# Performance work log

Hardware: AMD Instinct MI355X
Metric: run time of the kernel (lower is better)

Reference implementation:

```python
import jax, jax.numpy as jnp
import numpy as np

B, D = 4096, 512
N_PROTO = 1000          # prototype tasks
CLS_PER_TASK = 10       # indices*10 block size in original code
N_CLASSES = N_PROTO * CLS_PER_TASK
NUM_TEST = 10


def setup_inputs() -> dict:
    key = jax.random.key(0)
    k1, k2, k3 = jax.random.split(key, 3)
    img = jax.random.normal(k1, (B, D), dtype=jnp.float32)
    # image encoder output is L2-normalized and detached in the original
    image_features = img / jnp.linalg.norm(img, axis=-1, keepdims=True)
    ima_proto = jax.random.normal(k2, (N_PROTO, D), dtype=jnp.float32)
    ima_proto = ima_proto / jnp.linalg.norm(ima_proto, axis=-1, keepdims=True)
    text_features_raw = jax.random.normal(k3, (N_CLASSES, D), dtype=jnp.float32)
    logit_scale = jnp.asarray(np.log(1.0 / 0.07), dtype=jnp.float32)  # CLIP init
    return {
        "image_features": image_features,
        "ima_proto": ima_proto,
        "text_features_raw": text_features_raw,
        "logit_scale": logit_scale,
        "num_test": NUM_TEST,
    }


def reference(image_features, ima_proto, text_features_raw, logit_scale, num_test):
    n_proto = ima_proto.shape[0]
    n_classes = text_features_raw.shape[0]
    b = image_features.shape[0]
    k = min(int(num_test), n_proto)

    # probability = image_features @ ima_proto.t(); topk indices
    probability = image_features @ ima_proto.T                      # [B, n_proto]
    _, indices = jax.lax.top_k(probability, k)                      # [B, k]

    # text_features normalized, logit = image_features @ text_features.t()
    text_features = text_features_raw / jnp.linalg.norm(
        text_features_raw, axis=-1, keepdims=True)
    logit = image_features @ text_features.T                        # [B, n_classes]

    # vectorized form of the double loop:
    #   logits[j][idx*10 : idx*10+10] = logit[j][idx*10 : idx*10+10]
    sel = jnp.zeros((b, n_proto), dtype=logit.dtype)
    sel = sel.at[jnp.arange(b)[:, None], indices].set(1.0)          # [B, n_proto]
    block_of_class = jnp.arange(n_classes) // CLS_PER_TASK          # [n_classes]
    mask = sel[:, block_of_class]                                   # [B, n_classes]

    logits = jnp.exp(logit_scale) * (logit * mask)
    return logits
```

## Files before the change

kernel.cpp:

```cpp
#include <hip/hip_runtime.h>
#include <cfloat>
#include <math.h>

#define B_ROWS   4096
#define DIM      512
#define NPROTO   1000
#define NCLASSES 10000
#define KSEL     10
#define KCAND    12
#define CAP      256
#define PROB_LD  1024

#define PROB_BYTES 8388608u
#define OUT_BYTES  163840000u
#define ZHI_N4     ((OUT_BYTES - PROB_BYTES) / 16)
#define ZQ1        6000000u
#define ZS1        0u
#define ZQ2        (ZHI_N4 - ZQ1)
#define ZS2        ZQ1

#define GBM 64
#define GBN 128
#define GBK 32
#define ALD 40

typedef short s16x8 __attribute__((ext_vector_type(8)));
typedef float f32x4 __attribute__((ext_vector_type(4)));

static __device__ __forceinline__ unsigned short f2bf(float f) {
  unsigned int x = __float_as_uint(f);
  return (unsigned short)((x + 0x7fffu + ((x >> 16) & 1u)) >> 16);
}
static __device__ __forceinline__ s16x8 cvt8(float4 a, float4 b) {
  s16x8 r;
  r[0]=f2bf(a.x); r[1]=f2bf(a.y); r[2]=f2bf(a.z); r[3]=f2bf(a.w);
  r[4]=f2bf(b.x); r[5]=f2bf(b.y); r[6]=f2bf(b.z); r[7]=f2bf(b.w);
  return r;
}
static __device__ __forceinline__ unsigned short f2h(float f) {
  _Float16 h = (_Float16)f;
  return __builtin_bit_cast(unsigned short, h);
}

static __device__ __forceinline__ unsigned mono16(unsigned h) {
  return (h & 0x8000u) ? (~h & 0xffffu) : (h | 0x8000u);
}

static __device__ __forceinline__ void zero_share(
    f32x4* __restrict__ zhi, unsigned start, unsigned count,
    unsigned gth, unsigned nthreads)
{
  const f32x4 z4 = (f32x4)0.f;
  for (unsigned i = start + gth; i < start + count; i += nthreads)
    __builtin_nontemporal_store(z4, zhi + i);
}

__global__ __launch_bounds__(256) void k_gemm(
    const float* __restrict__ img, const float* __restrict__ proto,
    unsigned short* __restrict__ prob, f32x4* __restrict__ zhi,
    int* __restrict__ counts)
{
  __shared__ short Al[GBM * ALD];
  __shared__ short Bl[GBN * ALD];

  const int tid  = threadIdx.x;
  const int lane = tid & 63, wave = tid >> 6;
  const int wr = wave >> 1, wc = wave & 1;
  const int row0 = blockIdx.x * GBM;
  const int col0 = blockIdx.y * GBN;
  const unsigned gth = (blockIdx.y * gridDim.x + blockIdx.x) * 256 + tid;

  const int sr = tid >> 2;
  const int sc = (tid & 3) * 8;

  int pa = col0 + sr;      if (pa > NPROTO - 1) pa = NPROTO - 1;
  int pb = col0 + 64 + sr; if (pb > NPROTO - 1) pb = NPROTO - 1;
  const float* gA  = img   + (size_t)(row0 + sr) * DIM + sc;
  const float* gB0 = proto + (size_t)pa * DIM + sc;
  const float* gB1 = proto + (size_t)pb * DIM + sc;

  float4 ra0  = *(const float4*)(gA);      float4 ra1  = *(const float4*)(gA + 4);
  float4 rb00 = *(const float4*)(gB0);     float4 rb01 = *(const float4*)(gB0 + 4);
  float4 rb10 = *(const float4*)(gB1);     float4 rb11 = *(const float4*)(gB1 + 4);

  f32x4 acc[2][4];
#pragma unroll
  for (int m = 0; m < 2; ++m)
#pragma unroll
    for (int n = 0; n < 4; ++n) acc[m][n] = (f32x4)0.f;

  const int kg = lane >> 4;
  const int fr = lane & 15;

  for (int kt = 0; kt < DIM / GBK; ++kt) {
    *(s16x8*)&Al[sr * ALD + sc]        = cvt8(ra0, ra1);
    *(s16x8*)&Bl[sr * ALD + sc]        = cvt8(rb00, rb01);
    *(s16x8*)&Bl[(64 + sr) * ALD + sc] = cvt8(rb10, rb11);
    __syncthreads();

    if (kt + 1 < DIM / GBK) {
      const int k0 = (kt + 1) * GBK;
      ra0  = *(const float4*)(gA + k0);   ra1  = *(const float4*)(gA + k0 + 4);
      rb00 = *(const float4*)(gB0 + k0);  rb01 = *(const float4*)(gB0 + k0 + 4);
      rb10 = *(const float4*)(gB1 + k0);  rb11 = *(const float4*)(gB1 + k0 + 4);
    }

    s16x8 af[2], bf[4];
#pragma unroll
    for (int m = 0; m < 2; ++m)
      af[m] = *(const s16x8*)&Al[(wr * 32 + m * 16 + fr) * ALD + kg * 8];
#pragma unroll
    for (int n = 0; n < 4; ++n)
      bf[n] = *(const s16x8*)&Bl[(wc * 64 + n * 16 + fr) * ALD + kg * 8];
#pragma unroll
    for (int m = 0; m < 2; ++m)
#pragma unroll
      for (int n = 0; n < 4; ++n)
        acc[m][n] = __builtin_amdgcn_mfma_f32_16x16x32_bf16(
            af[m], bf[n], acc[m][n], 0, 0, 0);
    __syncthreads();
  }

#pragma unroll
  for (int m = 0; m < 2; ++m)
#pragma unroll
    for (int n = 0; n < 4; ++n) {
      const int r = row0 + wr * 32 + m * 16 + (lane >> 4) * 4;
      const int c = col0 + wc * 64 + n * 16 + fr;
#pragma unroll
      for (int reg = 0; reg < 4; ++reg)
        prob[(size_t)(r + reg) * PROB_LD + c] = f2h(acc[m][n][reg]);
    }

  if (blockIdx.x == 0 && blockIdx.y == 0)
    for (int i = tid; i < NPROTO; i += 256) counts[i] = 0;

  zero_share(zhi, ZS1, ZQ1, gth, 512 * 256);
}

__global__ __launch_bounds__(256) void k_select(
    unsigned short* __restrict__ prob, const float* __restrict__ img,
    const float* __restrict__ proto, int* __restrict__ counts,
    int* __restrict__ buckets, f32x4* __restrict__ zhi)
{
  const int tid  = threadIdx.x;
  const int wave = tid >> 6, lane = tid & 63;
  const int row  = blockIdx.x * 4 + wave;

  unsigned cand[16];
  {
    const uint4* pu = reinterpret_cast<const uint4*>(
        prob + (size_t)row * PROB_LD) + lane * 2;
    const uint4 w0 = pu[0], w1 = pu[1];
    const unsigned w[8] = {w0.x, w0.y, w0.z, w0.w, w1.x, w1.y, w1.z, w1.w};
    const int cbase = lane * 16;
#pragma unroll
    for (int r = 0; r < 8; ++r) {
      const int c0 = cbase + r * 2;
      const unsigned lo = w[r] & 0xffffu, hi = w[r] >> 16;
      cand[r * 2]     = (c0     < NPROTO) ? ((mono16(lo) << 16) | (0xffffu - c0))       : 0u;
      cand[r * 2 + 1] = (c0 + 1 < NPROTO) ? ((mono16(hi) << 16) | (0xffffu - (c0 + 1))) : 0u;
    }
  }

  int ci[KCAND];
#pragma unroll
  for (int kk = 0; kk < KCAND; ++kk) {
    unsigned best = cand[0];
#pragma unroll
    for (int r = 1; r < 16; ++r) best = max(best, cand[r]);
#pragma unroll
    for (int off = 32; off; off >>= 1)
      best = max(best, (unsigned)__shfl_xor((int)best, off));
    ci[kk] = 0xffff - (int)(best & 0xffffu);
#pragma unroll
    for (int r = 0; r < 16; ++r)
      if (cand[r] == best) cand[r] = 0u;
  }

  {
    const f32x4 z4 = (f32x4)0.f;
    f32x4* prow = reinterpret_cast<f32x4*>(prob + (size_t)row * PROB_LD);
    __builtin_nontemporal_store(z4, prow + lane);
    __builtin_nontemporal_store(z4, prow + 64 + lane);
  }

  const float4* a4 = reinterpret_cast<const float4*>(img + (size_t)row * DIM);
  const float4 a0 = a4[lane], a1 = a4[64 + lane];
  float dv[KCAND];
#pragma unroll
  for (int j = 0; j < KCAND; ++j) {
    const float4* p4 = reinterpret_cast<const float4*>(proto + (size_t)ci[j] * DIM);
    const float4 b0 = p4[lane], b1 = p4[64 + lane];
    float s = 0.f;
    s = fmaf(a0.x, b0.x, s); s = fmaf(a0.y, b0.y, s);
    s = fmaf(a0.z, b0.z, s); s = fmaf(a0.w, b0.w, s);
    s = fmaf(a1.x, b1.x, s); s = fmaf(a1.y, b1.y, s);
    s = fmaf(a1.z, b1.z, s); s = fmaf(a1.w, b1.w, s);
#pragma unroll
    for (int off = 32; off; off >>= 1) s += __shfl_xor(s, off);
    dv[j] = s;
  }

  unsigned picked = 0;
  for (int kk = 0; kk < KSEL; ++kk) {
    float bv = -FLT_MAX;
    int   bj = 0;
#pragma unroll
    for (int j = 0; j < KCAND; ++j)
      if (!((picked >> j) & 1u) && dv[j] > bv) { bv = dv[j]; bj = j; }
    picked |= 1u << bj;
    if (lane == kk) {
      const int pp  = ci[bj];
      const int pos = atomicAdd(&counts[pp], 1);
      if (pos < CAP) buckets[pp * CAP + pos] = row;
    }
  }

  zero_share(zhi, ZS2, ZQ2, blockIdx.x * 256 + tid, 1024 * 256);
}

__global__ __launch_bounds__(256) void k_compute(
    const float* __restrict__ img, const float* __restrict__ text,
    const int* __restrict__ counts, const int* __restrict__ buckets,
    const float* __restrict__ logit_scale, float* __restrict__ out)
{
  __shared__ float stext[KSEL * DIM];
  __shared__ float sfac[KSEL];

  const int p    = blockIdx.x;
  const int tid  = threadIdx.x;
  const int wave = tid >> 6, lane = tid & 63;

  {
    const float4* src = reinterpret_cast<const float4*>(text + (size_t)p * KSEL * DIM);
    float4* dst = reinterpret_cast<float4*>(stext);
#pragma unroll
    for (int i = 0; i < 5; ++i) dst[tid + i * 256] = src[tid + i * 256];
  }
  __syncthreads();

  const float scale = expf(logit_scale[0]);
#pragma unroll
  for (int j = wave; j < KSEL; j += 4) {
    const float4* t4 = reinterpret_cast<const float4*>(stext + j * DIM);
    float4 v0 = t4[lane], v1 = t4[64 + lane];
    float s = 0.f;
    s = fmaf(v0.x, v0.x, s); s = fmaf(v0.y, v0.y, s);
    s = fmaf(v0.z, v0.z, s); s = fmaf(v0.w, v0.w, s);
    s = fmaf(v1.x, v1.x, s); s = fmaf(v1.y, v1.y, s);
    s = fmaf(v1.z, v1.z, s); s = fmaf(v1.w, v1.w, s);
#pragma unroll
    for (int off = 32; off; off >>= 1) s += __shfl_down(s, off);
    if (lane == 0) sfac[j] = scale / sqrtf(s);
  }
  __syncthreads();

  const int n = min(counts[p], CAP);
  const float4* st4 = reinterpret_cast<const float4*>(stext);
  const int* bkt = buckets + p * CAP;

  int row = -1, nrow;
  float4 a0, a1, na0, na1;
  if (wave < n) {
    row = bkt[wave];
    const float4* a4 = reinterpret_cast<const float4*>(img + (size_t)row * DIM);
    a0 = a4[lane]; a1 = a4[64 + lane];
  }

  for (int i = wave; i < n; i += 4) {
    const int inext = i + 4;
    if (inext < n) {
      nrow = bkt[inext];
      const float4* a4 = reinterpret_cast<const float4*>(img + (size_t)nrow * DIM);
      na0 = a4[lane]; na1 = a4[64 + lane];
    }

    float acc[KSEL];
#pragma unroll
    for (int j = 0; j < KSEL; ++j) {
      const float4 b0 = st4[j * 128 + lane];
      const float4 b1 = st4[j * 128 + 64 + lane];
      float s = 0.f;
      s = fmaf(a0.x, b0.x, s); s = fmaf(a0.y, b0.y, s);
      s = fmaf(a0.z, b0.z, s); s = fmaf(a0.w, b0.w, s);
      s = fmaf(a1.x, b1.x, s); s = fmaf(a1.y, b1.y, s);
      s = fmaf(a1.z, b1.z, s); s = fmaf(a1.w, b1.w, s);
      acc[j] = s;
    }
#pragma unroll
    for (int j = 0; j < KSEL; ++j) {
#pragma unroll
      for (int off = 32; off; off >>= 1)
        acc[j] += __shfl_xor(acc[j], off);
    }
    float v = acc[0];
#pragma unroll
    for (int j = 1; j < KSEL; ++j) if (lane == j) v = acc[j];
    if (lane < KSEL)
      out[(size_t)row * NCLASSES + p * KSEL + lane] = v * sfac[lane];

    row = nrow; a0 = na0; a1 = na1;
  }
}

extern "C" void kernel_launch(void* const* d_in, const int* in_sizes, int n_in,
                              void* d_out, int out_size, void* d_ws, size_t ws_size,
                              hipStream_t stream) {
  const float* img    = (const float*)d_in[0];
  const float* proto  = (const float*)d_in[1];
  const float* text   = (const float*)d_in[2];
  const float* lscale = (const float*)d_in[3];

  unsigned short* prob = (unsigned short*)d_out;
  f32x4*  zhi  = (f32x4*)((char*)d_out + PROB_BYTES);
  float*  out  = (float*)d_out;

  int* counts  = (int*)d_ws;
  int* buckets = (int*)((char*)d_ws + 4096);

  k_gemm<<<dim3(B_ROWS / GBM, 1024 / GBN), 256, 0, stream>>>(
      img, proto, prob, zhi, counts);
  k_select<<<B_ROWS / 4, 256, 0, stream>>>(prob, img, proto, counts, buckets, zhi);
  k_compute<<<NPROTO, 256, 0, stream>>>(img, text, counts, buckets, lscale, out);
}
```

Baseline: 99.41 us.

## Fuse prototype GEMM with top-k candidate selection, pre-convert prototypes to bf16

Adds a prep kernel that converts the prototypes to bf16 into a padded workspace buffer and zeroes the counts. The GEMM and top-k selection are merged into one kernel: each 16-row block computes all 1024 prototype scores with MFMA, picks per-wave candidates in registers, merges them through LDS, then reranks in fp32 and fills the buckets. This removes the fp16 probability round-trip through the output buffer and the separate select launch. In exchange each block reads the full bf16 prototype matrix from global/L2 without LDS staging, only 256 blocks are launched, and zeroing the output moves into this one kernel.

```diff
diff --git a/kernel.cpp b/kernel.cpp
--- a/kernel.cpp
+++ b/kernel.cpp
@@ -5,24 +5,13 @@
 #define B_ROWS   4096
 #define DIM      512
 #define NPROTO   1000
+#define NPROTO_P 1024
 #define NCLASSES 10000
 #define KSEL     10
 #define KCAND    12
 #define CAP      256
-#define PROB_LD  1024
-
-#define PROB_BYTES 8388608u
-#define OUT_BYTES  163840000u
-#define ZHI_N4     ((OUT_BYTES - PROB_BYTES) / 16)
-#define ZQ1        6000000u
-#define ZS1        0u
-#define ZQ2        (ZHI_N4 - ZQ1)
-#define ZS2        ZQ1
-
-#define GBM 64
-#define GBN 128
-#define GBK 32
-#define ALD 40
+
+#define OUT_N4   10240000u
 
 typedef short s16x8 __attribute__((ext_vector_type(8)));
 typedef float f32x4 __attribute__((ext_vector_type(4)));
@@ -37,187 +26,156 @@
   r[4]=f2bf(b.x); r[5]=f2bf(b.y); r[6]=f2bf(b.z); r[7]=f2bf(b.w);
   return r;
 }
-static __device__ __forceinline__ unsigned short f2h(float f) {
+static __device__ __forceinline__ unsigned f2h(float f) {
   _Float16 h = (_Float16)f;
-  return __builtin_bit_cast(unsigned short, h);
-}
-
+  return (unsigned)__builtin_bit_cast(unsigned short, h);
+}
 static __device__ __forceinline__ unsigned mono16(unsigned h) {
   return (h & 0x8000u) ? (~h & 0xffffu) : (h | 0x8000u);
 }
 
 static __device__ __forceinline__ void zero_share(
-    f32x4* __restrict__ zhi, unsigned start, unsigned count,
+    f32x4* __restrict__ z, unsigned start, unsigned count,
     unsigned gth, unsigned nthreads)
 {
   const f32x4 z4 = (f32x4)0.f;
   for (unsigned i = start + gth; i < start + count; i += nthreads)
-    __builtin_nontemporal_store(z4, zhi + i);
-}
-
-__global__ __launch_bounds__(256) void k_gemm(
+    __builtin_nontemporal_store(z4, z + i);
+}
+
+__global__ __launch_bounds__(256) void k_prep(
+    const float* __restrict__ proto, short* __restrict__ protb,
+    int* __restrict__ counts)
+{
+  const int u = blockIdx.x * 256 + threadIdx.x;
+  s16x8 r = (s16x8)0;
+  if (u * 8 < NPROTO * DIM) {
+    const float4* s = reinterpret_cast<const float4*>(proto) + (size_t)u * 2;
+    r = cvt8(s[0], s[1]);
+  }
+  *reinterpret_cast<s16x8*>(protb + (size_t)u * 8) = r;
+  if (blockIdx.x == 0)
+    for (int i = threadIdx.x; i < NPROTO; i += 256) counts[i] = 0;
+}
+
+__global__ __launch_bounds__(512) void k_fused(
     const float* __restrict__ img, const float* __restrict__ proto,
-    unsigned short* __restrict__ prob, f32x4* __restrict__ zhi,
-    int* __restrict__ counts)
-{
-  __shared__ short Al[GBM * ALD];
-  __shared__ short Bl[GBN * ALD];
-
-  const int tid  = threadIdx.x;
-  const int lane = tid & 63, wave = tid >> 6;
-  const int wr = wave >> 1, wc = wave & 1;
-  const int row0 = blockIdx.x * GBM;
-  const int col0 = blockIdx.y * GBN;
-  const unsigned gth = (blockIdx.y * gridDim.x + blockIdx.x) * 256 + tid;
-
-  const int sr = tid >> 2;
-  const int sc = (tid & 3) * 8;
-
-  int pa = col0 + sr;      if (pa > NPROTO - 1) pa = NPROTO - 1;
-  int pb = col0 + 64 + sr; if (pb > NPROTO - 1) pb = NPROTO - 1;
-  const float* gA  = img   + (size_t)(row0 + sr) * DIM + sc;
-  const float* gB0 = proto + (size_t)pa * DIM + sc;
-  const float* gB1 = proto + (size_t)pb * DIM + sc;
-
-  float4 ra0  = *(const float4*)(gA);      float4 ra1  = *(const float4*)(gA + 4);
-  float4 rb00 = *(const float4*)(gB0);     float4 rb01 = *(const float4*)(gB0 + 4);
-  float4 rb10 = *(const float4*)(gB1);     float4 rb11 = *(const float4*)(gB1 + 4);
-
-  f32x4 acc[2][4];
-#pragma unroll
-  for (int m = 0; m < 2; ++m)
-#pragma unroll
-    for (int n = 0; n < 4; ++n) acc[m][n] = (f32x4)0.f;
-
-  const int kg = lane >> 4;
-  const int fr = lane & 15;
-
-  for (int kt = 0; kt < DIM / GBK; ++kt) {
-    *(s16x8*)&Al[sr * ALD + sc]        = cvt8(ra0, ra1);
-    *(s16x8*)&Bl[sr * ALD + sc]        = cvt8(rb00, rb01);
-    *(s16x8*)&Bl[(64 + sr) * ALD + sc] = cvt8(rb10, rb11);
-    __syncthreads();
-
-    if (kt + 1 < DIM / GBK) {
-      const int k0 = (kt + 1) * GBK;
-      ra0  = *(const float4*)(gA + k0);   ra1  = *(const float4*)(gA + k0 + 4);
-      rb00 = *(const float4*)(gB0 + k0);  rb01 = *(const float4*)(gB0 + k0 + 4);
-      rb10 = *(const float4*)(gB1 + k0);  rb11 = *(const float4*)(gB1 + k0 + 4);
-    }
-
-    s16x8 af[2], bf[4];
-#pragma unroll
-    for (int m = 0; m < 2; ++m)
-      af[m] = *(const s16x8*)&Al[(wr * 32 + m * 16 + fr) * ALD + kg * 8];
-#pragma unroll
-    for (int n = 0; n < 4; ++n)
-      bf[n] = *(const s16x8*)&Bl[(wc * 64 + n * 16 + fr) * ALD + kg * 8];
-#pragma unroll
-    for (int m = 0; m < 2; ++m)
-#pragma unroll
-      for (int n = 0; n < 4; ++n)
-        acc[m][n] = __builtin_amdgcn_mfma_f32_16x16x32_bf16(
-            af[m], bf[n], acc[m][n], 0, 0, 0);
-    __syncthreads();
-  }
-
-#pragma unroll
-  for (int m = 0; m < 2; ++m)
-#pragma unroll
-    for (int n = 0; n < 4; ++n) {
-      const int r = row0 + wr * 32 + m * 16 + (lane >> 4) * 4;
-      const int c = col0 + wc * 64 + n * 16 + fr;
-#pragma unroll
-      for (int reg = 0; reg < 4; ++reg)
-        prob[(size_t)(r + reg) * PROB_LD + c] = f2h(acc[m][n][reg]);
-    }
-
-  if (blockIdx.x == 0 && blockIdx.y == 0)
-    for (int i = tid; i < NPROTO; i += 256) counts[i] = 0;
-
-  zero_share(zhi, ZS1, ZQ1, gth, 512 * 256);
-}
-
-__global__ __launch_bounds__(256) void k_select(
-    unsigned short* __restrict__ prob, const float* __restrict__ img,
-    const float* __restrict__ proto, int* __restrict__ counts,
-    int* __restrict__ buckets, f32x4* __restrict__ zhi)
-{
+    const short* __restrict__ protb, int* __restrict__ counts,
+    int* __restrict__ buckets, f32x4* __restrict__ outz)
+{
+  __shared__ short A_lds[64 * 128];
+  __shared__ unsigned pool[16][8][KCAND];
+
   const int tid  = threadIdx.x;
   const int wave = tid >> 6, lane = tid & 63;
-  const int row  = blockIdx.x * 4 + wave;
-
-  unsigned cand[16];
+  const int kg = lane >> 4, fr = lane & 15;
+  const int row0 = blockIdx.x * 16;
+
   {
-    const uint4* pu = reinterpret_cast<const uint4*>(
-        prob + (size_t)row * PROB_LD) + lane * 2;
-    const uint4 w0 = pu[0], w1 = pu[1];
-    const unsigned w[8] = {w0.x, w0.y, w0.z, w0.w, w1.x, w1.y, w1.z, w1.w};
-    const int cbase = lane * 16;
-#pragma unroll
-    for (int r = 0; r < 8; ++r) {
-      const int c0 = cbase + r * 2;
-      const unsigned lo = w[r] & 0xffffu, hi = w[r] >> 16;
-      cand[r * 2]     = (c0     < NPROTO) ? ((mono16(lo) << 16) | (0xffffu - c0))       : 0u;
-      cand[r * 2 + 1] = (c0 + 1 < NPROTO) ? ((mono16(hi) << 16) | (0xffffu - (c0 + 1))) : 0u;
-    }
-  }
-
-  int ci[KCAND];
-#pragma unroll
-  for (int kk = 0; kk < KCAND; ++kk) {
-    unsigned best = cand[0];
-#pragma unroll
-    for (int r = 1; r < 16; ++r) best = max(best, cand[r]);
-#pragma unroll
-    for (int off = 32; off; off >>= 1)
-      best = max(best, (unsigned)__shfl_xor((int)best, off));
-    ci[kk] = 0xffff - (int)(best & 0xffffu);
-#pragma unroll
-    for (int r = 0; r < 16; ++r)
-      if (cand[r] == best) cand[r] = 0u;
-  }
-
-  {
-    const f32x4 z4 = (f32x4)0.f;
-    f32x4* prow = reinterpret_cast<f32x4*>(prob + (size_t)row * PROB_LD);
-    __builtin_nontemporal_store(z4, prow + lane);
-    __builtin_nontemporal_store(z4, prow + 64 + lane);
-  }
-
-  const float4* a4 = reinterpret_cast<const float4*>(img + (size_t)row * DIM);
-  const float4 a0 = a4[lane], a1 = a4[64 + lane];
-  float dv[KCAND];
-#pragma unroll
-  for (int j = 0; j < KCAND; ++j) {
-    const float4* p4 = reinterpret_cast<const float4*>(proto + (size_t)ci[j] * DIM);
-    const float4 b0 = p4[lane], b1 = p4[64 + lane];
-    float s = 0.f;
-    s = fmaf(a0.x, b0.x, s); s = fmaf(a0.y, b0.y, s);
-    s = fmaf(a0.z, b0.z, s); s = fmaf(a0.w, b0.w, s);
-    s = fmaf(a1.x, b1.x, s); s = fmaf(a1.y, b1.y, s);
-    s = fmaf(a1.z, b1.z, s); s = fmaf(a1.w, b1.w, s);
-#pragma unroll
-    for (int off = 32; off; off >>= 1) s += __shfl_xor(s, off);
-    dv[j] = s;
-  }
-
-  unsigned picked = 0;
-  for (int kk = 0; kk < KSEL; ++kk) {
-    float bv = -FLT_MAX;
-    int   bj = 0;
-#pragma unroll
-    for (int j = 0; j < KCAND; ++j)
-      if (!((picked >> j) & 1u) && dv[j] > bv) { bv = dv[j]; bj = j; }
-    picked |= 1u << bj;
-    if (lane == kk) {
-      const int pp  = ci[bj];
-      const int pos = atomicAdd(&counts[pp], 1);
-      if (pos < CAP) buckets[pp * CAP + pos] = row;
-    }
-  }
-
-  zero_share(zhi, ZS2, ZQ2, blockIdx.x * 256 + tid, 1024 * 256);
+    const int row = tid & 15, kc = tid >> 4;
+    const float4* s = reinterpret_cast<const float4*>(
+        img + (size_t)(row0 + row) * DIM + kc * 16);
+    float4 v0 = s[0], v1 = s[1], v2 = s[2], v3 = s[3];
+    *(s16x8*)&A_lds[(kc * 2    ) * 128 + row * 8] = cvt8(v0, v1);
+    *(s16x8*)&A_lds[(kc * 2 + 1) * 128 + row * 8] = cvt8(v2, v3);
+  }
+  __syncthreads();
+
+  const short* pb = protb + (size_t)(wave * 128 + fr) * DIM + kg * 8;
+
+  f32x4 acc[8];
+#pragma unroll
+  for (int f = 0; f < 8; ++f) acc[f] = (f32x4)0.f;
+
+#pragma unroll
+  for (int kt = 0; kt < DIM / 32; ++kt) {
+    s16x8 bf[8];
+#pragma unroll
+    for (int f = 0; f < 8; ++f)
+      bf[f] = *(const s16x8*)(pb + (size_t)f * 16 * DIM + kt * 32);
+    const s16x8 af = *(const s16x8*)&A_lds[(kt * 4 + kg) * 128 + fr * 8];
+#pragma unroll
+    for (int f = 0; f < 8; ++f)
+      acc[f] = __builtin_amdgcn_mfma_f32_16x16x32_bf16(af, bf[f], acc[f], 0, 0, 0);
+  }
+
+#pragma unroll
+  for (int reg = 0; reg < 4; ++reg) {
+    const int row = kg * 4 + reg;
+    unsigned pv[8];
+#pragma unroll
+    for (int f = 0; f < 8; ++f) {
+      const int col = wave * 128 + f * 16 + fr;
+      pv[f] = (col < NPROTO)
+            ? ((mono16(f2h(acc[f][reg])) << 16) | (0xffffu - col)) : 0u;
+    }
+    for (int kk = 0; kk < KCAND; ++kk) {
+      unsigned best = pv[0];
+#pragma unroll
+      for (int f = 1; f < 8; ++f) best = max(best, pv[f]);
+#pragma unroll
+      for (int off = 1; off < 16; off <<= 1)
+        best = max(best, (unsigned)__shfl_xor((int)best, off));
+      if (fr == kk) pool[row][wave][kk] = best;
+#pragma unroll
+      for (int f = 0; f < 8; ++f)
+        if (pv[f] == best) pv[f] = 0u;
+    }
+  }
+  __syncthreads();
+
+  for (int rr = 0; rr < 2; ++rr) {
+    const int r    = wave * 2 + rr;
+    const int grow = row0 + r;
+    const unsigned* pl = &pool[r][0][0];
+    unsigned c0 = pl[lane];
+    unsigned c1 = (lane < 32) ? pl[64 + lane] : 0u;
+
+    int ci[KCAND];
+    for (int kk = 0; kk < KCAND; ++kk) {
+      unsigned best = max(c0, c1);
+#pragma unroll
+      for (int off = 32; off; off >>= 1)
+        best = max(best, (unsigned)__shfl_xor((int)best, off));
+      ci[kk] = 0xffff - (int)(best & 0xffffu);
+      if (c0 == best) c0 = 0u;
+      if (c1 == best) c1 = 0u;
+    }
+
+    const float4* a4 = reinterpret_cast<const float4*>(img + (size_t)grow * DIM);
+    const float4 a0 = a4[lane], a1 = a4[64 + lane];
+    float dv[KCAND];
+#pragma unroll
+    for (int j = 0; j < KCAND; ++j) {
+      const float4* p4 = reinterpret_cast<const float4*>(proto + (size_t)ci[j] * DIM);
+      const float4 b0 = p4[lane], b1 = p4[64 + lane];
+      float s = 0.f;
+      s = fmaf(a0.x, b0.x, s); s = fmaf(a0.y, b0.y, s);
+      s = fmaf(a0.z, b0.z, s); s = fmaf(a0.w, b0.w, s);
+      s = fmaf(a1.x, b1.x, s); s = fmaf(a1.y, b1.y, s);
+      s = fmaf(a1.z, b1.z, s); s = fmaf(a1.w, b1.w, s);
+#pragma unroll
+      for (int off = 32; off; off >>= 1) s += __shfl_xor(s, off);
+      dv[j] = s;
+    }
+
+    unsigned picked = 0;
+    for (int kk = 0; kk < KSEL; ++kk) {
+      float bv = -FLT_MAX;
+      int   bj = 0;
+#pragma unroll
+      for (int j = 0; j < KCAND; ++j)
+        if (!((picked >> j) & 1u) && dv[j] > bv) { bv = dv[j]; bj = j; }
+      picked |= 1u << bj;
+      if (lane == kk) {
+        const int pp  = ci[bj];
+        const int pos = atomicAdd(&counts[pp], 1);
+        if (pos < CAP) buckets[pp * CAP + pos] = grow;
+      }
+    }
+  }
+
+  zero_share(outz, 0, OUT_N4, blockIdx.x * 512 + tid, 256 * 512);
 }
 
 __global__ __launch_bounds__(256) void k_compute(
@@ -312,15 +270,14 @@
   const float* text   = (const float*)d_in[2];
   const float* lscale = (const float*)d_in[3];
 
-  unsigned short* prob = (unsigned short*)d_out;
-  f32x4*  zhi  = (f32x4*)((char*)d_out + PROB_BYTES);
   float*  out  = (float*)d_out;
-
-  int* counts  = (int*)d_ws;
-  int* buckets = (int*)((char*)d_ws + 4096);
-
-  k_gemm<<<dim3(B_ROWS / GBM, 1024 / GBN), 256, 0, stream>>>(
-      img, proto, prob, zhi, counts);
-  k_select<<<B_ROWS / 4, 256, 0, stream>>>(prob, img, proto, counts, buckets, zhi);
+  f32x4*  outz = (f32x4*)d_out;
+
+  int*   counts  = (int*)d_ws;
+  int*   buckets = (int*)((char*)d_ws + 4096);
+  short* protb   = (short*)((char*)d_ws + 1048576);
+
+  k_prep<<<256, 256, 0, stream>>>(proto, protb, counts);
+  k_fused<<<256, 512, 0, stream>>>(img, proto, protb, counts, buckets, outz);
   k_compute<<<NPROTO, 256, 0, stream>>>(img, text, counts, buckets, lscale, out);
 }
```

Result: slower. 139.0 us (+39.9%).

## Fuse per-tile top-12 candidate selection into GEMM epilogue, drop fp16 prob matrix

Applied to the files above, without the earlier changes.

The GEMM epilogue now reduces each 64-column half-tile to its top-12 packed (value, index) candidates with wave shuffles and writes them to workspace, instead of storing the full fp16 probability matrix. The select kernel then reads 192 candidates per row rather than 1024 halves. Because the prob matrix no longer lives in the output buffer, the output zeroing covers the whole buffer uniformly, with no separate re-zeroing of the prob region. This cuts memory traffic and select work in exchange for a serial 12-round shuffle reduction in the GEMM epilogue.

```diff
diff --git a/kernel.cpp b/kernel.cpp
--- a/kernel.cpp
+++ b/kernel.cpp
@@ -8,16 +8,12 @@
 #define NCLASSES 10000
 #define KSEL     10
 #define KCAND    12
+#define NHALF    16
 #define CAP      256
-#define PROB_LD  1024
-
-#define PROB_BYTES 8388608u
-#define OUT_BYTES  163840000u
-#define ZHI_N4     ((OUT_BYTES - PROB_BYTES) / 16)
-#define ZQ1        6000000u
-#define ZS1        0u
-#define ZQ2        (ZHI_N4 - ZQ1)
-#define ZS2        ZQ1
+
+#define OUT_N4   10240000u
+#define ZQ1      6144000u
+#define ZQ2      (OUT_N4 - ZQ1)
 
 #define GBM 64
 #define GBN 128
@@ -37,27 +33,26 @@
   r[4]=f2bf(b.x); r[5]=f2bf(b.y); r[6]=f2bf(b.z); r[7]=f2bf(b.w);
   return r;
 }
-static __device__ __forceinline__ unsigned short f2h(float f) {
+static __device__ __forceinline__ unsigned f2h(float f) {
   _Float16 h = (_Float16)f;
-  return __builtin_bit_cast(unsigned short, h);
-}
-
+  return (unsigned)__builtin_bit_cast(unsigned short, h);
+}
 static __device__ __forceinline__ unsigned mono16(unsigned h) {
   return (h & 0x8000u) ? (~h & 0xffffu) : (h | 0x8000u);
 }
 
 static __device__ __forceinline__ void zero_share(
-    f32x4* __restrict__ zhi, unsigned start, unsigned count,
+    f32x4* __restrict__ z, unsigned start, unsigned count,
     unsigned gth, unsigned nthreads)
 {
   const f32x4 z4 = (f32x4)0.f;
   for (unsigned i = start + gth; i < start + count; i += nthreads)
-    __builtin_nontemporal_store(z4, zhi + i);
+    __builtin_nontemporal_store(z4, z + i);
 }
 
 __global__ __launch_bounds__(256) void k_gemm(
     const float* __restrict__ img, const float* __restrict__ proto,
-    unsigned short* __restrict__ prob, f32x4* __restrict__ zhi,
+    unsigned* __restrict__ cand, f32x4* __restrict__ outz,
     int* __restrict__ counts)
 {
   __shared__ short Al[GBM * ALD];
@@ -121,68 +116,62 @@
     __syncthreads();
   }
 
+  const int half = blockIdx.y * 2 + wc;
 #pragma unroll
   for (int m = 0; m < 2; ++m)
 #pragma unroll
-    for (int n = 0; n < 4; ++n) {
-      const int r = row0 + wr * 32 + m * 16 + (lane >> 4) * 4;
-      const int c = col0 + wc * 64 + n * 16 + fr;
-#pragma unroll
-      for (int reg = 0; reg < 4; ++reg)
-        prob[(size_t)(r + reg) * PROB_LD + c] = f2h(acc[m][n][reg]);
+    for (int reg = 0; reg < 4; ++reg) {
+      const int grow = row0 + wr * 32 + m * 16 + kg * 4 + reg;
+      unsigned pv[4];
+#pragma unroll
+      for (int n = 0; n < 4; ++n) {
+        const int col = col0 + wc * 64 + n * 16 + fr;
+        pv[n] = (col < NPROTO)
+              ? ((mono16(f2h(acc[m][n][reg])) << 16) | (0xffffu - col)) : 0u;
+      }
+      unsigned* cp = cand + (size_t)grow * (NHALF * KCAND) + half * KCAND;
+      for (int kk = 0; kk < KCAND; ++kk) {
+        unsigned best = max(max(pv[0], pv[1]), max(pv[2], pv[3]));
+#pragma unroll
+        for (int off = 1; off < 16; off <<= 1)
+          best = max(best, (unsigned)__shfl_xor((int)best, off));
+        if (fr == kk) cp[kk] = best;
+#pragma unroll
+        for (int n = 0; n < 4; ++n)
+          if (pv[n] == best) pv[n] = 0u;
+      }
     }
 
   if (blockIdx.x == 0 && blockIdx.y == 0)
     for (int i = tid; i < NPROTO; i += 256) counts[i] = 0;
 
-  zero_share(zhi, ZS1, ZQ1, gth, 512 * 256);
+  zero_share(outz, 0, ZQ1, gth, 512 * 256);
 }
 
 __global__ __launch_bounds__(256) void k_select(
-    unsigned short* __restrict__ prob, const float* __restrict__ img,
+    const unsigned* __restrict__ cand, const float* __restrict__ img,
     const float* __restrict__ proto, int* __restrict__ counts,
-    int* __restrict__ buckets, f32x4* __restrict__ zhi)
+    int* __restrict__ buckets, f32x4* __restrict__ outz)
 {
   const int tid  = threadIdx.x;
   const int wave = tid >> 6, lane = tid & 63;
   const int row  = blockIdx.x * 4 + wave;
 
-  unsigned cand[16];
-  {
-    const uint4* pu = reinterpret_cast<const uint4*>(
-        prob + (size_t)row * PROB_LD) + lane * 2;
-    const uint4 w0 = pu[0], w1 = pu[1];
-    const unsigned w[8] = {w0.x, w0.y, w0.z, w0.w, w1.x, w1.y, w1.z, w1.w};
-    const int cbase = lane * 16;
-#pragma unroll
-    for (int r = 0; r < 8; ++r) {
-      const int c0 = cbase + r * 2;
-      const unsigned lo = w[r] & 0xffffu, hi = w[r] >> 16;
-      cand[r * 2]     = (c0     < NPROTO) ? ((mono16(lo) << 16) | (0xffffu - c0))       : 0u;
-      cand[r * 2 + 1] = (c0 + 1 < NPROTO) ? ((mono16(hi) << 16) | (0xffffu - (c0 + 1))) : 0u;
-    }
-  }
+  const unsigned* pl = cand + (size_t)row * (NHALF * KCAND);
+  unsigned c0 = pl[lane];
+  unsigned c1 = pl[64 + lane];
+  unsigned c2 = pl[128 + lane];
 
   int ci[KCAND];
-#pragma unroll
   for (int kk = 0; kk < KCAND; ++kk) {
-    unsigned best = cand[0];
-#pragma unroll
-    for (int r = 1; r < 16; ++r) best = max(best, cand[r]);
+    unsigned best = max(c0, max(c1, c2));
 #pragma unroll
     for (int off = 32; off; off >>= 1)
       best = max(best, (unsigned)__shfl_xor((int)best, off));
     ci[kk] = 0xffff - (int)(best & 0xffffu);
-#pragma unroll
-    for (int r = 0; r < 16; ++r)
-      if (cand[r] == best) cand[r] = 0u;
-  }
-
-  {
-    const f32x4 z4 = (f32x4)0.f;
-    f32x4* prow = reinterpret_cast<f32x4*>(prob + (size_t)row * PROB_LD);
-    __builtin_nontemporal_store(z4, prow + lane);
-    __builtin_nontemporal_store(z4, prow + 64 + lane);
+    if (c0 == best) c0 = 0u;
+    if (c1 == best) c1 = 0u;
+    if (c2 == best) c2 = 0u;
   }
 
   const float4* a4 = reinterpret_cast<const float4*>(img + (size_t)row * DIM);
@@ -217,7 +206,7 @@
     }
   }
 
-  zero_share(zhi, ZS2, ZQ2, blockIdx.x * 256 + tid, 1024 * 256);
+  zero_share(outz, ZQ1, ZQ2, blockIdx.x * 256 + tid, 1024 * 256);
 }
 
 __global__ __launch_bounds__(256) void k_compute(
@@ -312,15 +301,16 @@
   const float* text   = (const float*)d_in[2];
   const float* lscale = (const float*)d_in[3];
 
-  unsigned short* prob = (unsigned short*)d_out;
-  f32x4*  zhi  = (f32x4*)((char*)d_out + PROB_BYTES);
   float*  out  = (float*)d_out;
-
-  int* counts  = (int*)d_ws;
-  int* buckets = (int*)((char*)d_ws + 4096);
+  f32x4*  outz = (f32x4*)d_out;
+
+  int*      counts  = (int*)d_ws;
+  int*      buckets = (int*)((char*)d_ws + 4096);
+  unsigned* cand    = (unsigned*)((char*)d_ws + 4096 + 1048576);
 
   k_gemm<<<dim3(B_ROWS / GBM, 1024 / GBN), 256, 0, stream>>>(
-      img, proto, prob, zhi, counts);
-  k_select<<<B_ROWS / 4, 256, 0, stream>>>(prob, img, proto, counts, buckets, zhi);
+      img, proto, cand, outz, counts);
+  k_select<<<B_ROWS / 4, 256, 0, stream>>>(
+      cand, img, proto, counts, buckets, outz);
   k_compute<<<NPROTO, 256, 0, stream>>>(img, text, counts, buckets, lscale, out);
 }
```

After: 116.2 us. +16.9%, slower.

## Pre-convert image features to bf16 and double-buffer GEMM shared tiles

Applied to the files above, without the earlier changes.

Adds a prep kernel that converts the image features to bf16 once into workspace and also zeroes the counts. The GEMM then loads bf16 A tiles directly instead of converting fp32 on every tile, and uses double-buffered LDS so one __syncthreads per k-step can be dropped. The compute kernel reads the bf16 image rows, halving its gather traffic. The trade-offs are an extra kernel launch and lower precision in the final logits, which are now computed from bf16 image features.

```diff
diff --git a/kernel.cpp b/kernel.cpp
--- a/kernel.cpp
+++ b/kernel.cpp
@@ -25,6 +25,7 @@
 #define ALD 40
 
 typedef short s16x8 __attribute__((ext_vector_type(8)));
+typedef short s16x4 __attribute__((ext_vector_type(4)));
 typedef float f32x4 __attribute__((ext_vector_type(4)));
 
 static __device__ __forceinline__ unsigned short f2bf(float f) {
@@ -41,27 +42,39 @@
   _Float16 h = (_Float16)f;
   return __builtin_bit_cast(unsigned short, h);
 }
-
+static __device__ __forceinline__ float bf2f(short v) {
+  return __uint_as_float(((unsigned)(unsigned short)v) << 16);
+}
 static __device__ __forceinline__ unsigned mono16(unsigned h) {
   return (h & 0x8000u) ? (~h & 0xffffu) : (h | 0x8000u);
 }
 
 static __device__ __forceinline__ void zero_share(
-    f32x4* __restrict__ zhi, unsigned start, unsigned count,
+    f32x4* __restrict__ z, unsigned start, unsigned count,
     unsigned gth, unsigned nthreads)
 {
   const f32x4 z4 = (f32x4)0.f;
   for (unsigned i = start + gth; i < start + count; i += nthreads)
-    __builtin_nontemporal_store(z4, zhi + i);
+    __builtin_nontemporal_store(z4, z + i);
+}
+
+__global__ __launch_bounds__(256) void k_prep(
+    const float* __restrict__ img, short* __restrict__ imgb,
+    int* __restrict__ counts)
+{
+  const int u = blockIdx.x * 256 + threadIdx.x;
+  const float4* s = reinterpret_cast<const float4*>(img) + (size_t)u * 2;
+  *reinterpret_cast<s16x8*>(imgb + (size_t)u * 8) = cvt8(s[0], s[1]);
+  if (blockIdx.x == 0)
+    for (int i = threadIdx.x; i < NPROTO; i += 256) counts[i] = 0;
 }
 
 __global__ __launch_bounds__(256) void k_gemm(
-    const float* __restrict__ img, const float* __restrict__ proto,
-    unsigned short* __restrict__ prob, f32x4* __restrict__ zhi,
-    int* __restrict__ counts)
-{
-  __shared__ short Al[GBM * ALD];
-  __shared__ short Bl[GBN * ALD];
+    const short* __restrict__ imgb, const float* __restrict__ proto,
+    unsigned short* __restrict__ prob, f32x4* __restrict__ outz)
+{
+  __shared__ short Al[2][GBM * ALD];
+  __shared__ short Bl[2][GBN * ALD];
 
   const int tid  = threadIdx.x;
   const int lane = tid & 63, wave = tid >> 6;
@@ -75,13 +88,13 @@
 
   int pa = col0 + sr;      if (pa > NPROTO - 1) pa = NPROTO - 1;
   int pb = col0 + 64 + sr; if (pb > NPROTO - 1) pb = NPROTO - 1;
-  const float* gA  = img   + (size_t)(row0 + sr) * DIM + sc;
+  const short* gA  = imgb  + (size_t)(row0 + sr) * DIM + sc;
   const float* gB0 = proto + (size_t)pa * DIM + sc;
   const float* gB1 = proto + (size_t)pb * DIM + sc;
 
-  float4 ra0  = *(const float4*)(gA);      float4 ra1  = *(const float4*)(gA + 4);
-  float4 rb00 = *(const float4*)(gB0);     float4 rb01 = *(const float4*)(gB0 + 4);
-  float4 rb10 = *(const float4*)(gB1);     float4 rb11 = *(const float4*)(gB1 + 4);
+  s16x8  ra   = *(const s16x8*)(gA);
+  float4 rb00 = *(const float4*)(gB0), rb01 = *(const float4*)(gB0 + 4);
+  float4 rb10 = *(const float4*)(gB1), rb11 = *(const float4*)(gB1 + 4);
 
   f32x4 acc[2][4];
 #pragma unroll
@@ -93,32 +106,32 @@
   const int fr = lane & 15;
 
   for (int kt = 0; kt < DIM / GBK; ++kt) {
-    *(s16x8*)&Al[sr * ALD + sc]        = cvt8(ra0, ra1);
-    *(s16x8*)&Bl[sr * ALD + sc]        = cvt8(rb00, rb01);
-    *(s16x8*)&Bl[(64 + sr) * ALD + sc] = cvt8(rb10, rb11);
-    __syncthreads();
+    const int cur = kt & 1;
+    *(s16x8*)&Al[cur][sr * ALD + sc]        = ra;
+    *(s16x8*)&Bl[cur][sr * ALD + sc]        = cvt8(rb00, rb01);
+    *(s16x8*)&Bl[cur][(64 + sr) * ALD + sc] = cvt8(rb10, rb11);
 
     if (kt + 1 < DIM / GBK) {
       const int k0 = (kt + 1) * GBK;
-      ra0  = *(const float4*)(gA + k0);   ra1  = *(const float4*)(gA + k0 + 4);
+      ra   = *(const s16x8*)(gA + k0);
       rb00 = *(const float4*)(gB0 + k0);  rb01 = *(const float4*)(gB0 + k0 + 4);
       rb10 = *(const float4*)(gB1 + k0);  rb11 = *(const float4*)(gB1 + k0 + 4);
     }
+    __syncthreads();
 
     s16x8 af[2], bf[4];
 #pragma unroll
     for (int m = 0; m < 2; ++m)
-      af[m] = *(const s16x8*)&Al[(wr * 32 + m * 16 + fr) * ALD + kg * 8];
+      af[m] = *(const s16x8*)&Al[cur][(wr * 32 + m * 16 + fr) * ALD + kg * 8];
 #pragma unroll
     for (int n = 0; n < 4; ++n)
-      bf[n] = *(const s16x8*)&Bl[(wc * 64 + n * 16 + fr) * ALD + kg * 8];
+      bf[n] = *(const s16x8*)&Bl[cur][(wc * 64 + n * 16 + fr) * ALD + kg * 8];
 #pragma unroll
     for (int m = 0; m < 2; ++m)
 #pragma unroll
       for (int n = 0; n < 4; ++n)
         acc[m][n] = __builtin_amdgcn_mfma_f32_16x16x32_bf16(
             af[m], bf[n], acc[m][n], 0, 0, 0);
-    __syncthreads();
   }
 
 #pragma unroll
@@ -132,16 +145,13 @@
         prob[(size_t)(r + reg) * PROB_LD + c] = f2h(acc[m][n][reg]);
     }
 
-  if (blockIdx.x == 0 && blockIdx.y == 0)
-    for (int i = tid; i < NPROTO; i += 256) counts[i] = 0;
-
-  zero_share(zhi, ZS1, ZQ1, gth, 512 * 256);
+  zero_share(outz, ZS1, ZQ1, gth, 512 * 256);
 }
 
 __global__ __launch_bounds__(256) void k_select(
     unsigned short* __restrict__ prob, const float* __restrict__ img,
     const float* __restrict__ proto, int* __restrict__ counts,
-    int* __restrict__ buckets, f32x4* __restrict__ zhi)
+    int* __restrict__ buckets, f32x4* __restrict__ outz)
 {
   const int tid  = threadIdx.x;
   const int wave = tid >> 6, lane = tid & 63;
@@ -217,11 +227,11 @@
     }
   }
 
-  zero_share(zhi, ZS2, ZQ2, blockIdx.x * 256 + tid, 1024 * 256);
+  zero_share(outz, ZS2, ZQ2, blockIdx.x * 256 + tid, 1024 * 256);
 }
 
 __global__ __launch_bounds__(256) void k_compute(
-    const float* __restrict__ img, const float* __restrict__ text,
+    const short* __restrict__ imgb, const float* __restrict__ text,
     const int* __restrict__ counts, const int* __restrict__ buckets,
     const float* __restrict__ logit_scale, float* __restrict__ out)
 {
@@ -261,20 +271,25 @@
   const int* bkt = buckets + p * CAP;
 
   int row = -1, nrow;
-  float4 a0, a1, na0, na1;
+  s16x4 r0, r1, nr0, nr1;
   if (wave < n) {
     row = bkt[wave];
-    const float4* a4 = reinterpret_cast<const float4*>(img + (size_t)row * DIM);
-    a0 = a4[lane]; a1 = a4[64 + lane];
+    const s16x4* ib = reinterpret_cast<const s16x4*>(imgb + (size_t)row * DIM);
+    r0 = ib[lane]; r1 = ib[64 + lane];
   }
 
   for (int i = wave; i < n; i += 4) {
     const int inext = i + 4;
     if (inext < n) {
       nrow = bkt[inext];
-      const float4* a4 = reinterpret_cast<const float4*>(img + (size_t)nrow * DIM);
-      na0 = a4[lane]; na1 = a4[64 + lane];
-    }
+      const s16x4* ib = reinterpret_cast<const s16x4*>(imgb + (size_t)nrow * DIM);
+      nr0 = ib[lane]; nr1 = ib[64 + lane];
+    }
+
+    const float ax0 = bf2f(r0[0]), ax1 = bf2f(r0[1]),
+                ax2 = bf2f(r0[2]), ax3 = bf2f(r0[3]);
+    const float ay0 = bf2f(r1[0]), ay1 = bf2f(r1[1]),
+                ay2 = bf2f(r1[2]), ay3 = bf2f(r1[3]);
 
     float acc[KSEL];
 #pragma unroll
@@ -282,10 +297,10 @@
       const float4 b0 = st4[j * 128 + lane];
       const float4 b1 = st4[j * 128 + 64 + lane];
       float s = 0.f;
-      s = fmaf(a0.x, b0.x, s); s = fmaf(a0.y, b0.y, s);
-      s = fmaf(a0.z, b0.z, s); s = fmaf(a0.w, b0.w, s);
-      s = fmaf(a1.x, b1.x, s); s = fmaf(a1.y, b1.y, s);
-      s = fmaf(a1.z, b1.z, s); s = fmaf(a1.w, b1.w, s);
+      s = fmaf(ax0, b0.x, s); s = fmaf(ax1, b0.y, s);
+      s = fmaf(ax2, b0.z, s); s = fmaf(ax3, b0.w, s);
+      s = fmaf(ay0, b1.x, s); s = fmaf(ay1, b1.y, s);
+      s = fmaf(ay2, b1.z, s); s = fmaf(ay3, b1.w, s);
       acc[j] = s;
     }
 #pragma unroll
@@ -300,7 +315,7 @@
     if (lane < KSEL)
       out[(size_t)row * NCLASSES + p * KSEL + lane] = v * sfac[lane];
 
-    row = nrow; a0 = na0; a1 = na1;
+    row = nrow; r0 = nr0; r1 = nr1;
   }
 }
 
@@ -313,14 +328,16 @@
   const float* lscale = (const float*)d_in[3];
 
   unsigned short* prob = (unsigned short*)d_out;
-  f32x4*  zhi  = (f32x4*)((char*)d_out + PROB_BYTES);
+  f32x4*  outz = (f32x4*)((char*)d_out + PROB_BYTES);
   float*  out  = (float*)d_out;
 
-  int* counts  = (int*)d_ws;
-  int* buckets = (int*)((char*)d_ws + 4096);
-
+  int*   counts  = (int*)d_ws;
+  int*   buckets = (int*)((char*)d_ws + 4096);
+  short* imgb    = (short*)((char*)d_ws + 4096 + 1048576);
+
+  k_prep<<<1024, 256, 0, stream>>>(img, imgb, counts);
   k_gemm<<<dim3(B_ROWS / GBM, 1024 / GBN), 256, 0, stream>>>(
-      img, proto, prob, zhi, counts);
-  k_select<<<B_ROWS / 4, 256, 0, stream>>>(prob, img, proto, counts, buckets, zhi);
-  k_compute<<<NPROTO, 256, 0, stream>>>(img, text, counts, buckets, lscale, out);
-}
+      imgb, proto, prob, outz);
+  k_select<<<B_ROWS / 4, 256, 0, stream>>>(prob, img, proto, counts, buckets, outz);
+  k_compute<<<NPROTO, 256, 0, stream>>>(imgb, text, counts, buckets, lscale, out);
+}
```

New measurement: 104.0 us. 4.6% more time.
